# Kernel optimization log

Hardware: AMD Instinct MI355X
Metric: run time of the kernel (lower is better)

## Reference

```python
import jax, jax.numpy as jnp
import numpy as np

BN_EPS = 1e-5

def _bn(x, gamma, beta):
    # BatchNorm1d in training mode: batch mean, biased variance
    m = jnp.mean(x, axis=0)
    v = jnp.var(x, axis=0)
    return (x - m) * jax.lax.rsqrt(v + BN_EPS) * gamma + beta

def setup_inputs() -> dict:
    key = jax.random.key(0)
    ks = jax.random.split(key, 12)
    N, E, D, ED = 50000, 600000, 128, 16
    s = lambda k, sh: jax.random.normal(k, sh, dtype=jnp.float32) * 0.05
    return {
        'h': jax.random.normal(ks[0], (N, D), dtype=jnp.float32),
        'edge_index': jax.random.randint(ks[1], (2, E), 0, N, dtype=jnp.int64),
        'edge_attr': jax.random.normal(ks[2], (E, ED), dtype=jnp.float32),
        'ee_w1': s(ks[3], (ED, D)), 'ee_b1': jnp.zeros((D,), jnp.float32),
        'ee_g1': jnp.ones((D,), jnp.float32), 'ee_bb1': jnp.zeros((D,), jnp.float32),
        'ee_w2': s(ks[4], (D, D)), 'ee_b2': jnp.zeros((D,), jnp.float32),
        'mlp_w1': s(ks[5], (D, D)), 'mlp_b1': jnp.zeros((D,), jnp.float32),
        'mlp_g1': jnp.ones((D,), jnp.float32), 'mlp_bb1': jnp.zeros((D,), jnp.float32),
        'mlp_w2': s(ks[6], (D, D)), 'mlp_b2': jnp.zeros((D,), jnp.float32),
        'mlp_g2': jnp.ones((D,), jnp.float32), 'mlp_bb2': jnp.zeros((D,), jnp.float32),
    }

def reference(h, edge_index, edge_attr, ee_w1, ee_b1, ee_g1, ee_bb1, ee_w2, ee_b2,
              mlp_w1, mlp_b1, mlp_g1, mlp_bb1, mlp_w2, mlp_b2, mlp_g2, mlp_bb2):
    N = h.shape[0]
    src, dst = edge_index[0], edge_index[1]
    # edge_encoder: Linear -> BN -> ReLU -> Linear
    e = jax.nn.relu(_bn(edge_attr @ ee_w1 + ee_b1, ee_g1, ee_bb1)) @ ee_w2 + ee_b2  # [E, D]
    # scatter-add edge embeddings to destination nodes
    agg_edge = jax.ops.segment_sum(e, dst, num_segments=N)  # [N, D]
    h = h + agg_edge
    # GINConv (eps=0): mlp(h + sum_{j->i} h_j)
    neigh = jax.ops.segment_sum(h[src], dst, num_segments=N)  # [N, D]
    z = h + neigh
    z = jax.nn.relu(_bn(z @ mlp_w1 + mlp_b1, mlp_g1, mlp_bb1))
    z = jax.nn.relu(_bn(z @ mlp_w2 + mlp_b2, mlp_g2, mlp_bb2))
    return z
```

## Files before the change

kernel.cpp:

```cpp
#include <hip/hip_runtime.h>
#include <hip/hip_bf16.h>

#define DD 128
#define EDIM 16

typedef short v8s __attribute__((ext_vector_type(8)));
typedef float v4f __attribute__((ext_vector_type(4)));

__device__ __forceinline__ float ldf(const void* p, int i, int bf){
  return bf ? __bfloat162float(((const __hip_bfloat16*)p)[i])
            : ((const float*)p)[i];
}
__device__ __forceinline__ float bfu_lo(unsigned u){
  unsigned b = (u & 0xffffu) << 16; float f; __builtin_memcpy(&f,&b,4); return f;
}
__device__ __forceinline__ float bfu_hi(unsigned u){
  unsigned b = u & 0xffff0000u; float f; __builtin_memcpy(&f,&b,4); return f;
}
__device__ __forceinline__ unsigned short f2bf(float f){
  unsigned u; __builtin_memcpy(&u,&f,4);
  unsigned r = (u + 0x7fffu + ((u>>16)&1u)) >> 16;
  return (unsigned short)r;
}
__device__ __forceinline__ unsigned packbf(float a, float b){
  return (unsigned)f2bf(a) | ((unsigned)f2bf(b) << 16);
}

__device__ __forceinline__ void load_attr_row(const void* __restrict__ attr,
                                              int e, int bf, float* a){
  if (bf){
    const uint4* ap = reinterpret_cast<const uint4*>(
        (const __hip_bfloat16*)attr + (size_t)e*EDIM);
    uint4 u0 = ap[0], u1 = ap[1];
    a[0]=bfu_lo(u0.x);  a[1]=bfu_hi(u0.x);  a[2]=bfu_lo(u0.y);  a[3]=bfu_hi(u0.y);
    a[4]=bfu_lo(u0.z);  a[5]=bfu_hi(u0.z);  a[6]=bfu_lo(u0.w);  a[7]=bfu_hi(u0.w);
    a[8]=bfu_lo(u1.x);  a[9]=bfu_hi(u1.x);  a[10]=bfu_lo(u1.y); a[11]=bfu_hi(u1.y);
    a[12]=bfu_lo(u1.z); a[13]=bfu_hi(u1.z); a[14]=bfu_lo(u1.w); a[15]=bfu_hi(u1.w);
  } else {
    const float4* ap = reinterpret_cast<const float4*>(
        (const float*)attr + (size_t)e*EDIM);
    float4 v0=ap[0], v1=ap[1], v2=ap[2], v3=ap[3];
    a[0]=v0.x; a[1]=v0.y; a[2]=v0.z; a[3]=v0.w;
    a[4]=v1.x; a[5]=v1.y; a[6]=v1.z; a[7]=v1.w;
    a[8]=v2.x; a[9]=v2.y; a[10]=v2.z; a[11]=v2.w;
    a[12]=v3.x;a[13]=v3.y;a[14]=v3.z; a[15]=v3.w;
  }
}

__global__ void k_detect(const void* g1, const int* ei, int E, int* flags){
  __shared__ int nz;
  if (threadIdx.x==0) nz = 0;
  __syncthreads();
  long long total = 2LL*E;
  long long stride = (total/1024) & ~1LL;
  if (stride < 2) stride = 2;
  long long idx = (long long)threadIdx.x*stride + 1;
  if (idx < total && ei[idx] != 0) atomicAdd(&nz, 1);
  __syncthreads();
  if (threadIdx.x==0){
    unsigned w = *(const unsigned*)g1;
    flags[0] = (w == 0x3F803F80u) ? 1 : 0;
    flags[1] = (nz == 0) ? 1 : 0;
  }
}

__global__ void k_transB(const void* w0, const void* w1, const void* w2,
                         const void* we1, const int* __restrict__ flags,
                         short* __restrict__ Bt){
  const int bf = flags[0];
  for (int idx = blockIdx.x*blockDim.x + threadIdx.x; idx < 3*16384 + 2048;
       idx += gridDim.x*blockDim.x){
    if (idx < 3*16384){
      int m = idx >> 14, r = idx & 16383;
      int nn = r >> 7, k = r & 127;
      const void* w = (m==0) ? w0 : ((m==1) ? w1 : w2);
      Bt[idx] = (short)f2bf(ldf(w, k*DD + nn, bf));
    } else {
      int r = idx - 3*16384;
      int nn = r >> 4, k = r & 15;
      Bt[idx] = (short)f2bf(ldf(we1, k*DD + nn, bf));
    }
  }
}

__global__ __launch_bounds__(256) void k_attr_moments(
    const void* __restrict__ attr, int E, const int* __restrict__ flags,
    float* __restrict__ Ssum , float* __restrict__ csum )
{
  __shared__ short Ws[4*512];
  __shared__ float sred[4][256];
  __shared__ float credu[4][16];
  const int t = threadIdx.x;
  const int wv = t >> 6, lane = t & 63, l15 = lane & 15, quad = lane >> 4;
  const int bf = flags[0];
  const int el = lane >> 1, half = lane & 1;
  short* W = &Ws[wv*512];

  v4f acc = (v4f){0.f,0.f,0.f,0.f};
  float cs[8];
  #pragma unroll
  for (int j=0;j<8;++j) cs[j]=0.f;

  const int nchunks = (E + 31) >> 5;
  for (int c = blockIdx.x*4 + wv; c < nchunks; c += gridDim.x*4){
    const int e = c*32 + el;
    const bool ok = (e < E);
    float f[8];
    if (bf){
      uint4 u = {0u,0u,0u,0u};
      if (ok) u = reinterpret_cast<const uint4*>(attr)[(size_t)e*2 + half];
      f[0]=bfu_lo(u.x); f[1]=bfu_hi(u.x); f[2]=bfu_lo(u.y); f[3]=bfu_hi(u.y);
      f[4]=bfu_lo(u.z); f[5]=bfu_hi(u.z); f[6]=bfu_lo(u.w); f[7]=bfu_hi(u.w);
    } else {
      float4 v0 = {0,0,0,0}, v1 = {0,0,0,0};
      if (ok){
        const float4* ap = reinterpret_cast<const float4*>(attr) +
                           (size_t)e*4 + half*2;
        v0 = ap[0]; v1 = ap[1];
      }
      f[0]=v0.x; f[1]=v0.y; f[2]=v0.z; f[3]=v0.w;
      f[4]=v1.x; f[5]=v1.y; f[6]=v1.z; f[7]=v1.w;
    }
    #pragma unroll
    for (int j=0;j<8;++j){
      cs[j] += f[j];
      W[(half*8 + j)*32 + el] = (short)f2bf(f[j]);
    }
    v8s a = *reinterpret_cast<const v8s*>(&W[l15*32 + quad*8]);
    acc = __builtin_amdgcn_mfma_f32_16x16x32_bf16(a, a, acc, 0,0,0);
  }

  #pragma unroll
  for (int r=0;r<4;++r) sred[wv][(quad*4 + r)*16 + l15] = acc[r];
  #pragma unroll
  for (int j=0;j<8;++j){
    #pragma unroll
    for (int off=2; off<64; off<<=1) cs[j] += __shfl_xor(cs[j], off, 64);
  }
  if (lane < 2){
    #pragma unroll
    for (int j=0;j<8;++j) credu[wv][lane*8 + j] = cs[j];
  }
  __syncthreads();
  float s = sred[0][t]+sred[1][t]+sred[2][t]+sred[3][t];
  atomicAdd(&Ssum[t], s);
  if (t < 16){
    float s2 = credu[0][t]+credu[1][t]+credu[2][t]+credu[3][t];
    atomicAdd(&csum[t], s2);
  }
}

__global__ void k_edge_bn(const void* __restrict__ w1, const void* __restrict__ g,
                          const void* __restrict__ bb,
                          const float* __restrict__ Ssum, const float* __restrict__ csum,
                          float Einv, const int* __restrict__ flags,
                          float* __restrict__ sc, float* __restrict__ sh){
  const int j = threadIdx.x;
  const int bf = flags[0];
  float w[EDIM];
  #pragma unroll
  for (int p=0;p<EDIM;++p) w[p] = ldf(w1, p*DD + j, bf);
  float mu0 = 0.f;
  #pragma unroll
  for (int p=0;p<EDIM;++p) mu0 += csum[p]*Einv*w[p];
  float s2 = 0.f;
  #pragma unroll
  for (int p=0;p<EDIM;++p){
    float acc = 0.f;
    #pragma unroll
    for (int q=0;q<EDIM;++q) acc += Ssum[p*16 + q]*w[q];
    s2 += w[p]*acc;
  }
  float var = s2*Einv - mu0*mu0;
  float scv = ldf(g, j, bf) * rsqrtf(var + 1e-5f);
  sc[j] = scv;
  sh[j] = ldf(bb, j, bf) - mu0*scv;
}

__global__ void k_hist(const int* __restrict__ ei, int E,
                       const int* __restrict__ flags, int* __restrict__ deg){
  const int i64 = flags[1];
  const int2* ei2 = (const int2*)ei;
  for (int e = blockIdx.x*blockDim.x + threadIdx.x; e < E;
       e += gridDim.x*blockDim.x){
    int d = i64 ? ei2[E + e].x : ei[E + e];
    atomicAdd(&deg[d], 1);
  }
}

__global__ void k_scan_partial(const int* __restrict__ deg, int n,
                               int* __restrict__ bsum){
  __shared__ int red[256];
  const int t = threadIdx.x;
  const int base = blockIdx.x*1024;
  int s = 0;
  for (int i = t; i < 1024; i += 256){
    int g = base + i;
    s += (g < n) ? deg[g] : 0;
  }
  red[t] = s; __syncthreads();
  for (int off=128; off>0; off>>=1){
    if (t < off) red[t] += red[t+off];
    __syncthreads();
  }
  if (t==0) bsum[blockIdx.x] = red[0];
}

__global__ void k_scan_tops(int* __restrict__ bsum, int nb, int* __restrict__ total){
  __shared__ int buf[256];
  const int t = threadIdx.x;
  int v = (t < nb) ? bsum[t] : 0;
  buf[t] = v; __syncthreads();
  for (int off=1; off<256; off<<=1){
    int x = (t>=off) ? buf[t-off] : 0;
    __syncthreads();
    buf[t] += x; __syncthreads();
  }
  if (t < nb) bsum[t] = buf[t] - v;
  if (t == 255) *total = buf[255];
}

__global__ void k_scan_final(const int* __restrict__ deg, int n,
                             const int* __restrict__ bsum, const int* __restrict__ total,
                             int* __restrict__ offsets, int* __restrict__ cursor){
  __shared__ int red[256];
  const int t = threadIdx.x;
  const int base = blockIdx.x*1024 + t*4;
  int v[4]; int s = 0;
  #pragma unroll
  for (int k=0;k<4;++k){
    int g = base + k;
    v[k] = (g < n) ? deg[g] : 0;
    s += v[k];
  }
  red[t] = s; __syncthreads();
  for (int off=1; off<256; off<<=1){
    int x = (t>=off) ? red[t-off] : 0;
    __syncthreads();
    red[t] += x; __syncthreads();
  }
  int ex = bsum[blockIdx.x] + red[t] - s;
  #pragma unroll
  for (int k=0;k<4;++k){
    int g = base + k;
    if (g < n){ offsets[g] = ex; cursor[g] = ex; }
    ex += v[k];
  }
  if (blockIdx.x==0 && t==0) offsets[n] = *total;
}

__global__ void k_scatter(const int* __restrict__ ei, const void* __restrict__ attr,
                          int E, const int* __restrict__ flags,
                          int* __restrict__ cursor, int* __restrict__ esrc,
                          int* __restrict__ snode, unsigned* __restrict__ attrpH){
  const int i64 = flags[1];
  const int bf = flags[0];
  const int2* ei2 = (const int2*)ei;
  for (int e = blockIdx.x*blockDim.x + threadIdx.x; e < E;
       e += gridDim.x*blockDim.x){
    int d = i64 ? ei2[E + e].x : ei[E + e];
    int s = i64 ? ei2[e].x     : ei[e];
    int pp = atomicAdd(&cursor[d], 1);
    esrc[pp] = s;
    snode[pp] = d;
    float a[EDIM];
    load_attr_row(attr, e, bf, a);
    uint4* dst = reinterpret_cast<uint4*>(attrpH + (size_t)pp*8);
    uint4 o0, o1;
    o0.x = packbf(a[0],a[1]);   o0.y = packbf(a[2],a[3]);
    o0.z = packbf(a[4],a[5]);   o0.w = packbf(a[6],a[7]);
    o1.x = packbf(a[8],a[9]);   o1.y = packbf(a[10],a[11]);
    o1.z = packbf(a[12],a[13]); o1.w = packbf(a[14],a[15]);
    dst[0] = o0; dst[1] = o1;
  }
}

__global__ __launch_bounds__(256) void k_edgeagg(
    const short* __restrict__ attrpH, const short* __restrict__ w1t,
    const float* __restrict__ sc, const float* __restrict__ sh,
    const int* __restrict__ offsets, const int* __restrict__ snode,
    int n, int E, float* __restrict__ Pagg)
{
  const int t = threadIdx.x;
  const int wv = t >> 6, lane = t & 63, l15 = lane & 15, quad = lane >> 4;
  const int W0 = blockIdx.x*64 + wv*16;
  if (W0 >= E) return;

  v8s a = (v8s){0,0,0,0,0,0,0,0};
  if (quad < 2){
    int slot = W0 + l15;
    if (slot < E)
      a = *reinterpret_cast<const v8s*>(&attrpH[(size_t)slot*EDIM + quad*8]);
  }
  float val[8][4];
  #pragma unroll
  for (int cg=0;cg<8;++cg){
    v8s b = (v8s){0,0,0,0,0,0,0,0};
    if (quad < 2)
      b = *reinterpret_cast<const v8s*>(&w1t[(cg*16+l15)*EDIM + quad*8]);
    v4f acc = (v4f){0.f,0.f,0.f,0.f};
    acc = __builtin_amdgcn_mfma_f32_16x16x32_bf16(a, b, acc, 0,0,0);
    const float scv = sc[cg*16+l15], shv = sh[cg*16+l15];
    #pragma unroll
    for (int reg=0;reg<4;++reg)
      val[cg][reg] = fmaxf(fmaf(acc[reg], scv, shv), 0.f);
  }

  int i = snode[W0];
  const int Wend = (W0 + 16 < E) ? (W0 + 16) : E;
  int segb = W0;
  while (segb < Wend && i < n){
    int oe = offsets[i+1];
    int sege = (oe < Wend) ? oe : Wend;
    if (sege > segb){
      float part[8];
      #pragma unroll
      for (int cg=0;cg<8;++cg) part[cg] = 0.f;
      #pragma unroll
      for (int reg=0;reg<4;++reg){
        int s = W0 + quad*4 + reg;
        if (s >= segb && s < sege){
          #pragma unroll
          for (int cg=0;cg<8;++cg) part[cg] += val[cg][reg];
        }
      }
      #pragma unroll
      for (int cg=0;cg<8;++cg){
        part[cg] += __shfl_xor(part[cg], 16, 64);
        part[cg] += __shfl_xor(part[cg], 32, 64);
      }
      if (quad == 0){
        #pragma unroll
        for (int cg=0;cg<8;++cg)
          atomicAdd(&Pagg[(size_t)i*DD + cg*16 + l15], part[cg]);
      }
      segb = sege;
    }
    ++i;
  }
}

__global__ __launch_bounds__(256) void k_gather_z(
    const uint4* __restrict__ hnew16, const int* __restrict__ offsets,
    const int* __restrict__ esrc, int n, uint4* __restrict__ zH16)
{
  const int wv = threadIdx.x >> 6, lane = threadIdx.x & 63;
  const int g = lane >> 4, c16 = lane & 15;
  for (int i = blockIdx.x*4 + wv; i < n; i += gridDim.x*4){
    const int beg = offsets[i], end = offsets[i+1];
    float a0=0.f,a1=0.f,a2=0.f,a3=0.f,a4=0.f,a5=0.f,a6=0.f,a7=0.f;
    int c0 = beg;
    for (; c0 + 8 <= end; c0 += 8){
      int s1 = esrc[c0 + g];
      int s2 = esrc[c0 + 4 + g];
      uint4 u = hnew16[(size_t)s1*16 + c16];
      uint4 v = hnew16[(size_t)s2*16 + c16];
      a0 += bfu_lo(u.x)+bfu_lo(v.x); a1 += bfu_hi(u.x)+bfu_hi(v.x);
      a2 += bfu_lo(u.y)+bfu_lo(v.y); a3 += bfu_hi(u.y)+bfu_hi(v.y);
      a4 += bfu_lo(u.z)+bfu_lo(v.z); a5 += bfu_hi(u.z)+bfu_hi(v.z);
      a6 += bfu_lo(u.w)+bfu_lo(v.w); a7 += bfu_hi(u.w)+bfu_hi(v.w);
    }
    for (; c0 < end; c0 += 4){
      int r = c0 + g;
      if (r < end){
        uint4 u = hnew16[(size_t)esrc[r]*16 + c16];
        a0 += bfu_lo(u.x); a1 += bfu_hi(u.x);
        a2 += bfu_lo(u.y); a3 += bfu_hi(u.y);
        a4 += bfu_lo(u.z); a5 += bfu_hi(u.z);
        a6 += bfu_lo(u.w); a7 += bfu_hi(u.w);
      }
    }
    a0 += __shfl_xor(a0,16,64); a1 += __shfl_xor(a1,16,64);
    a2 += __shfl_xor(a2,16,64); a3 += __shfl_xor(a3,16,64);
    a4 += __shfl_xor(a4,16,64); a5 += __shfl_xor(a5,16,64);
    a6 += __shfl_xor(a6,16,64); a7 += __shfl_xor(a7,16,64);
    a0 += __shfl_xor(a0,32,64); a1 += __shfl_xor(a1,32,64);
    a2 += __shfl_xor(a2,32,64); a3 += __shfl_xor(a3,32,64);
    a4 += __shfl_xor(a4,32,64); a5 += __shfl_xor(a5,32,64);
    a6 += __shfl_xor(a6,32,64); a7 += __shfl_xor(a7,32,64);
    if (lane < 16){
      uint4 m = hnew16[(size_t)i*16 + lane];
      uint4 o;
      o.x = packbf(a0+bfu_lo(m.x), a1+bfu_hi(m.x));
      o.y = packbf(a2+bfu_lo(m.y), a3+bfu_hi(m.y));
      o.z = packbf(a4+bfu_lo(m.z), a5+bfu_hi(m.z));
      o.w = packbf(a6+bfu_lo(m.w), a7+bfu_hi(m.w));
      zH16[(size_t)i*16 + lane] = o;
    }
  }
}

__global__ __launch_bounds__(256) void k_gemm_mfma(
    const short* __restrict__ A, const float* __restrict__ Af32,
    const short* __restrict__ Bt, const void* __restrict__ bias,
    const float* __restrict__ psc, const float* __restrict__ psh,
    const int* __restrict__ deg, const void* __restrict__ H,
    const int* __restrict__ flags, int n,
    __hip_bfloat16* __restrict__ out, float* __restrict__ stats, int mode)
{
  __shared__ float sb[256];
  const int t = threadIdx.x;
  const int bfi = flags[0];
  sb[t] = 0.f;
  __syncthreads();
  const int wv = t >> 6, lane = t & 63, l15 = lane & 15, quad = lane >> 4;
  const int R0 = blockIdx.x*64 + wv*16;

  v8s a[4];
  {
    const int arow = R0 + l15;
    const bool ok = (arow < n);
    #pragma unroll
    for (int ks=0;ks<4;++ks){
      const int k0 = ks*32 + quad*8;
      float f[8];
      if (Af32){
        float4 v0 = {0,0,0,0}, v1 = {0,0,0,0};
        if (ok){
          const float4* ap = reinterpret_cast<const float4*>(
              Af32 + (size_t)arow*DD + k0);
          v0 = ap[0]; v1 = ap[1];
        }
        f[0]=v0.x; f[1]=v0.y; f[2]=v0.z; f[3]=v0.w;
        f[4]=v1.x; f[5]=v1.y; f[6]=v1.z; f[7]=v1.w;
        v8s av;
        #pragma unroll
        for (int j=0;j<8;++j) av[j] = (short)f2bf(f[j]);
        a[ks] = av;
      } else {
        uint4 u = {0u,0u,0u,0u};
        if (ok) u = *reinterpret_cast<const uint4*>(&A[(size_t)arow*DD + k0]);
        if (psc){
          f[0]=bfu_lo(u.x); f[1]=bfu_hi(u.x); f[2]=bfu_lo(u.y); f[3]=bfu_hi(u.y);
          f[4]=bfu_lo(u.z); f[5]=bfu_hi(u.z); f[6]=bfu_lo(u.w); f[7]=bfu_hi(u.w);
          v8s av;
          #pragma unroll
          for (int j=0;j<8;++j)
            av[j] = (short)f2bf(fmaxf(fmaf(f[j], psc[k0+j], psh[k0+j]), 0.f));
          a[ks] = av;
        } else {
          a[ks] = *reinterpret_cast<v8s*>(&u);
        }
      }
    }
  }

  v4f acc[8];
  #pragma unroll
  for (int cg=0;cg<8;++cg) acc[cg] = (v4f){0.f,0.f,0.f,0.f};
  #pragma unroll
  for (int ks=0;ks<4;++ks){
    #pragma unroll
    for (int cg=0;cg<8;++cg){
      v8s b = *reinterpret_cast<const v8s*>(
                &Bt[(cg*16+l15)*DD + ks*32 + quad*8]);
      acc[cg] = __builtin_amdgcn_mfma_f32_16x16x32_bf16(a[ks], b, acc[cg], 0,0,0);
    }
  }

  float bc[8];
  #pragma unroll
  for (int cg=0;cg<8;++cg) bc[cg] = ldf(bias, cg*16 + l15, bfi);
  float ss[8], sq[8];
  #pragma unroll
  for (int cg=0;cg<8;++cg){ ss[cg]=0.f; sq[cg]=0.f; }

  #pragma unroll
  for (int reg=0;reg<4;++reg){
    const int row = R0 + quad*4 + reg;
    if (row < n){
      float degf = (mode==1) ? (float)deg[row] : 0.f;
      #pragma unroll
      for (int cg=0;cg<8;++cg){
        const int col = cg*16 + l15;
        float x = acc[cg][reg];
        if (mode==1) x = fmaf(degf, bc[cg], x) + ldf(H, (size_t)row*DD + col, bfi);
        else         x += bc[cg];
        out[(size_t)row*DD + col] = __float2bfloat16(x);
        ss[cg] += x; sq[cg] += x*x;
      }
    }
  }

  if (stats){
    #pragma unroll
    for (int cg=0;cg<8;++cg){
      float s = ss[cg], q = sq[cg];
      s += __shfl_xor(s, 16, 64); s += __shfl_xor(s, 32, 64);
      q += __shfl_xor(q, 16, 64); q += __shfl_xor(q, 32, 64);
      if (quad == 0){
        atomicAdd(&sb[cg*16 + l15], s);
        atomicAdd(&sb[128 + cg*16 + l15], q);
      }
    }
    __syncthreads();
    atomicAdd(&stats[t], sb[t]);
  }
}

__global__ void k_bn_params(const float* __restrict__ stats, const void* __restrict__ g,
                            const void* __restrict__ bb, const int* __restrict__ flags,
                            float inv_n, float* __restrict__ sc, float* __restrict__ sh){
  const int j = threadIdx.x;
  const int bf = flags[0];
  float mean = stats[j]*inv_n;
  float var  = stats[DD+j]*inv_n - mean*mean;
  float s = ldf(g, j, bf) * rsqrtf(var + 1e-5f);
  sc[j] = s;
  sh[j] = ldf(bb, j, bf) - mean*s;
}

__global__ void k_final(const unsigned* __restrict__ yH,
                        const float* __restrict__ sc, const float* __restrict__ sh,
                        int n, const int* __restrict__ flags, void* __restrict__ out){
  const int bf = flags[0];
  const int nw = n*64;
  for (int i = blockIdx.x*blockDim.x + threadIdx.x; i < nw;
       i += gridDim.x*blockDim.x){
    const int j0 = (i & 63)*2;
    unsigned u = yH[i];
    float v0 = fmaxf(fmaf(bfu_lo(u), sc[j0],   sh[j0]),   0.f);
    float v1 = fmaxf(fmaf(bfu_hi(u), sc[j0+1], sh[j0+1]), 0.f);
    if (bf){
      ((unsigned*)out)[i] = packbf(v0, v1);
    } else {
      *reinterpret_cast<float2*>((float*)out + 2*(size_t)i) = make_float2(v0, v1);
    }
  }
}

extern "C" void kernel_launch(void* const* d_in, const int* in_sizes, int n_in,
                              void* d_out, int out_size, void* d_ws, size_t ws_size,
                              hipStream_t stream)
{
  const void* h       = d_in[0];
  const int*  ei      = (const int*)d_in[1];
  const void* attr    = d_in[2];
  const void* ee_w1   = d_in[3];
  const void* ee_g1   = d_in[5];
  const void* ee_bb1  = d_in[6];
  const void* ee_w2   = d_in[7];
  const void* ee_b2   = d_in[8];
  const void* mlp_w1  = d_in[9];
  const void* mlp_b1  = d_in[10];
  const void* mlp_g1  = d_in[11];
  const void* mlp_bb1 = d_in[12];
  const void* mlp_w2  = d_in[13];
  const void* mlp_b2  = d_in[14];
  const void* mlp_g2  = d_in[15];
  const void* mlp_bb2 = d_in[16];

  const int N = in_sizes[0] / DD;
  const int E = in_sizes[1] / 2;
  const int nb = (N + 1023) / 1024;

  char* p = (char*)d_ws;
  auto alloc = [&](size_t bytes)->char*{
    char* r = p;
    p += (bytes + 255) & ~size_t(255);
    return r;
  };
  int* flags = (int*)alloc(8);
  char* zbase = p;
  int*   deg    = (int*)  zbase;
  float* csum   = (float*)(zbase + (size_t)N*4);
  float* Ssum   = (float*)(zbase + (size_t)N*4 + 64);
  float* stats1 = (float*)(zbase + (size_t)N*4 + 64 + 1024);
  float* stats2 = (float*)(zbase + (size_t)N*4 + 64 + 2048);
  float* Pagg   = (float*)(zbase + (size_t)N*4 + 64 + 3072);
  size_t zlen   = (size_t)N*4 + 64 + 3072 + (size_t)N*DD*4;
  p += (zlen + 255) & ~size_t(255);
  int*   bsum    = (int*)  alloc(256*4);
  int*   total   = (int*)  alloc(64);
  int*   offsets = (int*)  alloc((size_t)(N+1)*4);
  int*   cursor  = (int*)  alloc((size_t)N*4);
  int*   esrc    = (int*)  alloc((size_t)E*4);
  int*   snode   = (int*)  alloc((size_t)E*4);
  unsigned* attrpH = (unsigned*)alloc((size_t)E*EDIM*2);
  short* Bt      = (short*)alloc((size_t)(3*DD*DD + DD*EDIM)*2);
  short* w1t     = Bt + 3*DD*DD;
  float* ebn_sc  = (float*)alloc(512);
  float* ebn_sh  = (float*)alloc(512);
  float* sc1     = (float*)alloc(512);
  float* sh1     = (float*)alloc(512);
  float* sc2     = (float*)alloc(512);
  float* sh2     = (float*)alloc(512);
  short* hnewH   = (short*)alloc((size_t)N*DD*2);
  short* zH      = (short*)alloc((size_t)N*DD*2);
  short* y1H     = (short*)alloc((size_t)N*DD*2);
  short* y2H     = (short*)alloc((size_t)N*DD*2);
  (void)ws_size; (void)n_in; (void)out_size;

  const int g64  = (N + 63) / 64;
  const int e64  = (E + 63) / 64;
  const int gseg = (N + 15) / 16;

  hipMemsetAsync(zbase, 0, zlen, stream);
  k_detect<<<1, 1024, 0, stream>>>(ee_g1, ei, E, flags);
  k_transB<<<208, 256, 0, stream>>>(ee_w2, mlp_w1, mlp_w2, ee_w1, flags, Bt);
  k_attr_moments<<<256, 256, 0, stream>>>(attr, E, flags, Ssum, csum);
  k_edge_bn<<<1, 128, 0, stream>>>(ee_w1, ee_g1, ee_bb1, Ssum, csum,
                                   1.0f/(float)E, flags, ebn_sc, ebn_sh);
  k_hist<<<1024, 256, 0, stream>>>(ei, E, flags, deg);
  k_scan_partial<<<nb, 256, 0, stream>>>(deg, N, bsum);
  k_scan_tops<<<1, 256, 0, stream>>>(bsum, nb, total);
  k_scan_final<<<nb, 256, 0, stream>>>(deg, N, bsum, total, offsets, cursor);
  k_scatter<<<1024, 256, 0, stream>>>(ei, attr, E, flags, cursor, esrc,
                                      snode, attrpH);

  k_edgeagg<<<e64, 256, 0, stream>>>((const short*)attrpH, w1t, ebn_sc, ebn_sh,
                                     offsets, snode, N, E, Pagg);

  k_gemm_mfma<<<g64, 256, 0, stream>>>(nullptr, Pagg, Bt, ee_b2,
                                       nullptr, nullptr, deg, h, flags, N,
                                       (__hip_bfloat16*)hnewH, nullptr, 1);
  k_gather_z<<<gseg, 256, 0, stream>>>((const uint4*)hnewH, offsets, esrc, N,
                                       (uint4*)zH);
  k_gemm_mfma<<<g64, 256, 0, stream>>>(zH, nullptr, Bt + 16384, mlp_b1,
                                       nullptr, nullptr, nullptr, nullptr,
                                       flags, N, (__hip_bfloat16*)y1H, stats1, 0);
  k_bn_params<<<1, 128, 0, stream>>>(stats1, mlp_g1, mlp_bb1, flags,
                                     1.0f/(float)N, sc1, sh1);
  k_gemm_mfma<<<g64, 256, 0, stream>>>(y1H, nullptr, Bt + 32768, mlp_b2,
                                       sc1, sh1, nullptr, nullptr,
                                       flags, N, (__hip_bfloat16*)y2H, stats2, 0);
  k_bn_params<<<1, 128, 0, stream>>>(stats2, mlp_g2, mlp_bb2, flags,
                                     1.0f/(float)N, sc2, sh2);

  k_final<<<2048, 256, 0, stream>>>((const unsigned*)y2H, sc2, sh2,
                                    N, flags, d_out);
}
```

Before: 444.5 us.

## Gather edge attrs by permutation in edgeagg and reduce segments through shared memory

The scatter kernel no longer copies a permuted bf16 copy of edge attributes. It writes a packed (src, edge id) pair per sorted slot, and the edge aggregation kernel reads attributes indirectly through that id. Edge aggregation now stores post-BN ReLU activations for 64 edges in a 32 KB shared tile and reduces each destination segment per column. It uses plain stores for segments fully inside the block and atomics only for segments that cross a block boundary. A win2node table built during the scan gives each block its starting node. This trades the coalesced attribute read for a random gather and larger shared memory use, which lowers occupancy.

Result: no change. 453.3 us (+2.0%).

```diff
diff --git a/kernel.cpp b/kernel.cpp
--- a/kernel.cpp
+++ b/kernel.cpp
@@ -24,27 +24,6 @@
 }
 __device__ __forceinline__ unsigned packbf(float a, float b){
   return (unsigned)f2bf(a) | ((unsigned)f2bf(b) << 16);
-}
-
-__device__ __forceinline__ void load_attr_row(const void* __restrict__ attr,
-                                              int e, int bf, float* a){
-  if (bf){
-    const uint4* ap = reinterpret_cast<const uint4*>(
-        (const __hip_bfloat16*)attr + (size_t)e*EDIM);
-    uint4 u0 = ap[0], u1 = ap[1];
-    a[0]=bfu_lo(u0.x);  a[1]=bfu_hi(u0.x);  a[2]=bfu_lo(u0.y);  a[3]=bfu_hi(u0.y);
-    a[4]=bfu_lo(u0.z);  a[5]=bfu_hi(u0.z);  a[6]=bfu_lo(u0.w);  a[7]=bfu_hi(u0.w);
-    a[8]=bfu_lo(u1.x);  a[9]=bfu_hi(u1.x);  a[10]=bfu_lo(u1.y); a[11]=bfu_hi(u1.y);
-    a[12]=bfu_lo(u1.z); a[13]=bfu_hi(u1.z); a[14]=bfu_lo(u1.w); a[15]=bfu_hi(u1.w);
-  } else {
-    const float4* ap = reinterpret_cast<const float4*>(
-        (const float*)attr + (size_t)e*EDIM);
-    float4 v0=ap[0], v1=ap[1], v2=ap[2], v3=ap[3];
-    a[0]=v0.x; a[1]=v0.y; a[2]=v0.z; a[3]=v0.w;
-    a[4]=v1.x; a[5]=v1.y; a[6]=v1.z; a[7]=v1.w;
-    a[8]=v2.x; a[9]=v2.y; a[10]=v2.z; a[11]=v2.w;
-    a[12]=v3.x;a[13]=v3.y;a[14]=v3.z; a[15]=v3.w;
-  }
 }
 
 __global__ void k_detect(const void* g1, const int* ei, int E, int* flags){
@@ -222,7 +201,8 @@
 
 __global__ void k_scan_final(const int* __restrict__ deg, int n,
                              const int* __restrict__ bsum, const int* __restrict__ total,
-                             int* __restrict__ offsets, int* __restrict__ cursor){
+                             int* __restrict__ offsets, int* __restrict__ cursor,
+                             int* __restrict__ win2node){
   __shared__ int red[256];
   const int t = threadIdx.x;
   const int base = blockIdx.x*1024 + t*4;
@@ -243,56 +223,67 @@
   #pragma unroll
   for (int k=0;k<4;++k){
     int g = base + k;
-    if (g < n){ offsets[g] = ex; cursor[g] = ex; }
+    if (g < n){
+      offsets[g] = ex; cursor[g] = ex;
+      int end = ex + v[k];
+      for (int w = (ex + 63) >> 6; (w << 6) < end; ++w) win2node[w] = g;
+    }
     ex += v[k];
   }
   if (blockIdx.x==0 && t==0) offsets[n] = *total;
 }
 
-__global__ void k_scatter(const int* __restrict__ ei, const void* __restrict__ attr,
-                          int E, const int* __restrict__ flags,
-                          int* __restrict__ cursor, int* __restrict__ esrc,
-                          int* __restrict__ snode, unsigned* __restrict__ attrpH){
+__global__ void k_scatter(const int* __restrict__ ei, int E,
+                          const int* __restrict__ flags,
+                          int* __restrict__ cursor, int2* __restrict__ se){
   const int i64 = flags[1];
-  const int bf = flags[0];
   const int2* ei2 = (const int2*)ei;
   for (int e = blockIdx.x*blockDim.x + threadIdx.x; e < E;
        e += gridDim.x*blockDim.x){
     int d = i64 ? ei2[E + e].x : ei[E + e];
     int s = i64 ? ei2[e].x     : ei[e];
     int pp = atomicAdd(&cursor[d], 1);
-    esrc[pp] = s;
-    snode[pp] = d;
-    float a[EDIM];
-    load_attr_row(attr, e, bf, a);
-    uint4* dst = reinterpret_cast<uint4*>(attrpH + (size_t)pp*8);
-    uint4 o0, o1;
-    o0.x = packbf(a[0],a[1]);   o0.y = packbf(a[2],a[3]);
-    o0.z = packbf(a[4],a[5]);   o0.w = packbf(a[6],a[7]);
-    o1.x = packbf(a[8],a[9]);   o1.y = packbf(a[10],a[11]);
-    o1.z = packbf(a[12],a[13]); o1.w = packbf(a[14],a[15]);
-    dst[0] = o0; dst[1] = o1;
+    se[pp] = make_int2(s, e);
   }
 }
 
 __global__ __launch_bounds__(256) void k_edgeagg(
-    const short* __restrict__ attrpH, const short* __restrict__ w1t,
+    const void* __restrict__ attr, const int2* __restrict__ se,
+    const short* __restrict__ w1t,
     const float* __restrict__ sc, const float* __restrict__ sh,
-    const int* __restrict__ offsets, const int* __restrict__ snode,
-    int n, int E, float* __restrict__ Pagg)
+    const int* __restrict__ offsets, const int* __restrict__ win2node,
+    const int* __restrict__ flags, int n, int E, float* __restrict__ Pagg)
 {
+  __shared__ float Ps[64*DD];
   const int t = threadIdx.x;
   const int wv = t >> 6, lane = t & 63, l15 = lane & 15, quad = lane >> 4;
-  const int W0 = blockIdx.x*64 + wv*16;
-  if (W0 >= E) return;
+  const int bf = flags[0];
+  const int B0 = blockIdx.x * 64;
+  const int Bend = (B0 + 64 < E) ? (B0 + 64) : E;
+  const int W0 = B0 + wv*16;
 
   v8s a = (v8s){0,0,0,0,0,0,0,0};
   if (quad < 2){
     int slot = W0 + l15;
-    if (slot < E)
-      a = *reinterpret_cast<const v8s*>(&attrpH[(size_t)slot*EDIM + quad*8]);
-  }
-  float val[8][4];
+    if (slot < E){
+      int e = se[slot].y;
+      if (bf){
+        a = *reinterpret_cast<const v8s*>(
+              (const short*)attr + (size_t)e*EDIM + quad*8);
+      } else {
+        const float4* ap = reinterpret_cast<const float4*>(
+              (const float*)attr + (size_t)e*EDIM + quad*8);
+        float4 v0 = ap[0], v1 = ap[1];
+        v8s av;
+        av[0]=(short)f2bf(v0.x); av[1]=(short)f2bf(v0.y);
+        av[2]=(short)f2bf(v0.z); av[3]=(short)f2bf(v0.w);
+        av[4]=(short)f2bf(v1.x); av[5]=(short)f2bf(v1.y);
+        av[6]=(short)f2bf(v1.z); av[7]=(short)f2bf(v1.w);
+        a = av;
+      }
+    }
+  }
+  const int lr0 = wv*16 + quad*4;
   #pragma unroll
   for (int cg=0;cg<8;++cg){
     v8s b = (v8s){0,0,0,0,0,0,0,0};
@@ -303,46 +294,28 @@
     const float scv = sc[cg*16+l15], shv = sh[cg*16+l15];
     #pragma unroll
     for (int reg=0;reg<4;++reg)
-      val[cg][reg] = fmaxf(fmaf(acc[reg], scv, shv), 0.f);
-  }
-
-  int i = snode[W0];
-  const int Wend = (W0 + 16 < E) ? (W0 + 16) : E;
-  int segb = W0;
-  while (segb < Wend && i < n){
-    int oe = offsets[i+1];
-    int sege = (oe < Wend) ? oe : Wend;
-    if (sege > segb){
-      float part[8];
-      #pragma unroll
-      for (int cg=0;cg<8;++cg) part[cg] = 0.f;
-      #pragma unroll
-      for (int reg=0;reg<4;++reg){
-        int s = W0 + quad*4 + reg;
-        if (s >= segb && s < sege){
-          #pragma unroll
-          for (int cg=0;cg<8;++cg) part[cg] += val[cg][reg];
-        }
-      }
-      #pragma unroll
-      for (int cg=0;cg<8;++cg){
-        part[cg] += __shfl_xor(part[cg], 16, 64);
-        part[cg] += __shfl_xor(part[cg], 32, 64);
-      }
-      if (quad == 0){
-        #pragma unroll
-        for (int cg=0;cg<8;++cg)
-          atomicAdd(&Pagg[(size_t)i*DD + cg*16 + l15], part[cg]);
-      }
-      segb = sege;
-    }
-    ++i;
+      Ps[(lr0+reg)*DD + cg*16 + l15] = fmaxf(fmaf(acc[reg], scv, shv), 0.f);
+  }
+  __syncthreads();
+
+  const int c = t & 127, half = t >> 7;
+  const int i0 = win2node[blockIdx.x];
+  for (int idx = i0 + half; idx < n; idx += 2){
+    int nb = offsets[idx], ne = offsets[idx+1];
+    if (nb >= Bend) break;
+    int s0 = nb > B0 ? nb : B0;
+    int s1 = ne < Bend ? ne : Bend;
+    if (s1 <= s0) continue;
+    float sum = 0.f;
+    for (int s = s0; s < s1; ++s) sum += Ps[(s - B0)*DD + c];
+    if (nb < B0 || ne > Bend) atomicAdd(&Pagg[(size_t)idx*DD + c], sum);
+    else                      Pagg[(size_t)idx*DD + c] = sum;
   }
 }
 
 __global__ __launch_bounds__(256) void k_gather_z(
     const uint4* __restrict__ hnew16, const int* __restrict__ offsets,
-    const int* __restrict__ esrc, int n, uint4* __restrict__ zH16)
+    const int2* __restrict__ se, int n, uint4* __restrict__ zH16)
 {
   const int wv = threadIdx.x >> 6, lane = threadIdx.x & 63;
   const int g = lane >> 4, c16 = lane & 15;
@@ -351,8 +324,8 @@
     float a0=0.f,a1=0.f,a2=0.f,a3=0.f,a4=0.f,a5=0.f,a6=0.f,a7=0.f;
     int c0 = beg;
     for (; c0 + 8 <= end; c0 += 8){
-      int s1 = esrc[c0 + g];
-      int s2 = esrc[c0 + 4 + g];
+      int s1 = se[c0 + g].x;
+      int s2 = se[c0 + 4 + g].x;
       uint4 u = hnew16[(size_t)s1*16 + c16];
       uint4 v = hnew16[(size_t)s2*16 + c16];
       a0 += bfu_lo(u.x)+bfu_lo(v.x); a1 += bfu_hi(u.x)+bfu_hi(v.x);
@@ -363,7 +336,7 @@
     for (; c0 < end; c0 += 4){
       int r = c0 + g;
       if (r < end){
-        uint4 u = hnew16[(size_t)esrc[r]*16 + c16];
+        uint4 u = hnew16[(size_t)se[r].x*16 + c16];
         a0 += bfu_lo(u.x); a1 += bfu_hi(u.x);
         a2 += bfu_lo(u.y); a3 += bfu_hi(u.y);
         a4 += bfu_lo(u.z); a5 += bfu_hi(u.z);
@@ -553,6 +526,7 @@
   const int N = in_sizes[0] / DD;
   const int E = in_sizes[1] / 2;
   const int nb = (N + 1023) / 1024;
+  const int e64 = (E + 63) / 64;
 
   char* p = (char*)d_ws;
   auto alloc = [&](size_t bytes)->char*{
@@ -570,13 +544,12 @@
   float* Pagg   = (float*)(zbase + (size_t)N*4 + 64 + 3072);
   size_t zlen   = (size_t)N*4 + 64 + 3072 + (size_t)N*DD*4;
   p += (zlen + 255) & ~size_t(255);
-  int*   bsum    = (int*)  alloc(256*4);
-  int*   total   = (int*)  alloc(64);
-  int*   offsets = (int*)  alloc((size_t)(N+1)*4);
-  int*   cursor  = (int*)  alloc((size_t)N*4);
-  int*   esrc    = (int*)  alloc((size_t)E*4);
-  int*   snode   = (int*)  alloc((size_t)E*4);
-  unsigned* attrpH = (unsigned*)alloc((size_t)E*EDIM*2);
+  int*   bsum     = (int*)  alloc(256*4);
+  int*   total    = (int*)  alloc(64);
+  int*   offsets  = (int*)  alloc((size_t)(N+1)*4);
+  int*   cursor   = (int*)  alloc((size_t)N*4);
+  int*   win2node = (int*)  alloc((size_t)e64*4);
+  int2*  se       = (int2*) alloc((size_t)E*8);
   short* Bt      = (short*)alloc((size_t)(3*DD*DD + DD*EDIM)*2);
   short* w1t     = Bt + 3*DD*DD;
   float* ebn_sc  = (float*)alloc(512);
@@ -592,7 +565,6 @@
   (void)ws_size; (void)n_in; (void)out_size;
 
   const int g64  = (N + 63) / 64;
-  const int e64  = (E + 63) / 64;
   const int gseg = (N + 15) / 16;
 
   hipMemsetAsync(zbase, 0, zlen, stream);
@@ -604,17 +576,17 @@
   k_hist<<<1024, 256, 0, stream>>>(ei, E, flags, deg);
   k_scan_partial<<<nb, 256, 0, stream>>>(deg, N, bsum);
   k_scan_tops<<<1, 256, 0, stream>>>(bsum, nb, total);
-  k_scan_final<<<nb, 256, 0, stream>>>(deg, N, bsum, total, offsets, cursor);
-  k_scatter<<<1024, 256, 0, stream>>>(ei, attr, E, flags, cursor, esrc,
-                                      snode, attrpH);
-
-  k_edgeagg<<<e64, 256, 0, stream>>>((const short*)attrpH, w1t, ebn_sc, ebn_sh,
-                                     offsets, snode, N, E, Pagg);
+  k_scan_final<<<nb, 256, 0, stream>>>(deg, N, bsum, total, offsets, cursor,
+                                       win2node);
+  k_scatter<<<1024, 256, 0, stream>>>(ei, E, flags, cursor, se);
+
+  k_edgeagg<<<e64, 256, 0, stream>>>(attr, se, w1t, ebn_sc, ebn_sh,
+                                     offsets, win2node, flags, N, E, Pagg);
 
   k_gemm_mfma<<<g64, 256, 0, stream>>>(nullptr, Pagg, Bt, ee_b2,
                                        nullptr, nullptr, deg, h, flags, N,
                                        (__hip_bfloat16*)hnewH, nullptr, 1);
-  k_gather_z<<<gseg, 256, 0, stream>>>((const uint4*)hnewH, offsets, esrc, N,
+  k_gather_z<<<gseg, 256, 0, stream>>>((const uint4*)hnewH, offsets, se, N,
                                        (uint4*)zH);
   k_gemm_mfma<<<g64, 256, 0, stream>>>(zH, nullptr, Bt + 16384, mlp_b1,
                                        nullptr, nullptr, nullptr, nullptr,
```
